# Kernel tuning notes

Hardware: AMD Instinct MI355X
Metric: run time of the kernel (lower is better)

Reference implementation:

```python
import jax, jax.numpy as jnp
import numpy as np

B, C, H, W = 16, 256, 56, 56
G, K, R = 16, 3, 2
CR = C // R          # reduced channels = 128
KKG = K * K * G      # span output channels = 144
EPS = 1e-5


def setup_inputs() -> dict:
    key = jax.random.key(0)
    ks = jax.random.split(key, 5)
    return {
        "x": jax.random.normal(ks[0], (B, C, H, W), jnp.float32),
        "w_reduce": jax.random.normal(ks[1], (CR, C), jnp.float32) * 0.05,
        "b_reduce": jax.random.normal(ks[2], (CR,), jnp.float32) * 0.05,
        "gamma": jnp.ones((CR,), jnp.float32),
        "beta": jnp.zeros((CR,), jnp.float32),
        "w_span": jax.random.normal(ks[3], (KKG, CR), jnp.float32) * 0.05,
        "b_span": jax.random.normal(ks[4], (KKG,), jnp.float32) * 0.05,
    }


def _conv1x1(x, w, bias):
    # 1x1 conv == channel contraction
    return jnp.einsum('bchw,oc->bohw', x, w) + bias[None, :, None, None]


def _involution(x, w_reduce, b_reduce, gamma, beta, w_span, b_span):
    b, c, h, w = x.shape
    # kernel-generation branch: reduce -> BN (batch stats) -> ReLU -> span
    t = _conv1x1(x, w_reduce, b_reduce)
    mu = t.mean(axis=(0, 2, 3), keepdims=True)
    var = t.var(axis=(0, 2, 3), keepdims=True)  # biased, as torch BN training
    t = (t - mu) * jax.lax.rsqrt(var + EPS)
    t = t * gamma[None, :, None, None] + beta[None, :, None, None]
    t = jax.nn.relu(t)
    kern = _conv1x1(t, w_span, b_span)  # [b, k*k*g, h, w]
    # 'b (k j g) h w -> b g (k j) h w'
    kern = kern.reshape(b, K, K, G, h, w).transpose(0, 3, 1, 2, 4, 5)
    kern = kern.reshape(b, G, K * K, h, w)
    # unfold x into [b, g, d, k*k, h, w] via shifted padded slices (no dense im2col buffer write pattern beyond necessity)
    p = K // 2
    xp = jnp.pad(x, ((0, 0), (0, 0), (p, p), (p, p)))
    patches = jnp.stack(
        [xp[:, :, i:i + h, j:j + w] for i in range(K) for j in range(K)],
        axis=2)  # [b, c, k*k, h, w]
    patches = patches.reshape(b, G, c // G, K * K, h, w)
    out = jnp.einsum('bgdxhw,bgxhw->bgdhw', patches, kern)  # weighted window sum
    return out.reshape(b, c, h, w)


def reference(x, w_reduce, b_reduce, gamma, beta, w_span, b_span):
    return _involution(x, w_reduce, b_reduce, gamma, beta, w_span, b_span)
```

## Files before the change

### kernel.cpp

```cpp
#include <hip/hip_runtime.h>

#define B_   16
#define C_   256
#define HW_  3136
#define W_   56
#define CR_  128
#define KKG_ 144
#define G_   16
#define NPOS (B_*HW_)
#define EPS_ 1e-5f
#define NBLK 784

typedef float f32x4 __attribute__((ext_vector_type(4)));
typedef short s16x8 __attribute__((ext_vector_type(8)));
typedef short s16x4 __attribute__((ext_vector_type(4)));

#define T2_OFF_B    0
#define KERN_OFF_B  12845056
#define GP_OFF_B    27295744
#define STAT_OFF_B  28098560
#define WBFR_OFF_B  28099584
#define WBFS_OFF_B  28165120

__device__ inline unsigned short f2bf(float f) {
    unsigned u = __float_as_uint(f);
    u += 0x7fff + ((u >> 16) & 1);
    return (unsigned short)(u >> 16);
}
__device__ inline float bf2f(unsigned short h) {
    return __uint_as_float(((unsigned)h) << 16);
}

__global__ __launch_bounds__(256) void prep_cast(
    const float* __restrict__ w_reduce, const float* __restrict__ w_span,
    unsigned short* __restrict__ wbfr, unsigned short* __restrict__ wbfs)
{
    int idx = blockIdx.x * 256 + threadIdx.x;
    if (idx < 32768) {
        wbfr[idx] = f2bf(w_reduce[idx]);
    } else {
        int k = idx - 32768;
        if (k < 18432) wbfs[k] = f2bf(w_span[k]);
    }
}

__global__ __launch_bounds__(256) void reduce_mfma(
    const float* __restrict__ x, const unsigned short* __restrict__ wbfr,
    unsigned short* __restrict__ t2, float* __restrict__ gp)
{
    __shared__ __align__(16) short as_[128 * 40];
    __shared__ __align__(16) short bs_[64 * 40];
    __shared__ float redp[128][2], redq[128][2];

    const int tid = threadIdx.x;
    const int lane = tid & 63, wv = tid >> 6;
    const int q = lane >> 4, i = lane & 15;
    const int mrow = (wv >> 1) * 64, nrow = (wv & 1) * 32;
    const int blk = blockIdx.x;
    const int b = blk / 49;
    const int p0 = (blk % 49) * 64;

    const float* xb = x + (size_t)b * C_ * HW_ + p0;

    const int o_a = tid >> 1, half = tid & 1;
    const int cp = tid >> 4, rq = tid & 15;

    f32x4 acc[4][2] = {};

    for (int c0 = 0; c0 < C_; c0 += 32) {
        {
            const unsigned short* src = wbfr + o_a * C_ + c0 + half * 16;
            s16x8 w0 = *(const s16x8*)src;
            s16x8 w1 = *(const s16x8*)(src + 8);
            *(s16x8*)&as_[o_a * 40 + half * 16] = w0;
            *(s16x8*)&as_[o_a * 40 + half * 16 + 8] = w1;
        }
        {
            const float* s0 = xb + (size_t)(c0 + 2 * cp) * HW_ + rq * 4;
            float4 va = *(const float4*)s0;
            float4 vb = *(const float4*)(s0 + HW_);
            float a4[4] = {va.x, va.y, va.z, va.w};
            float b4[4] = {vb.x, vb.y, vb.z, vb.w};
            #pragma unroll
            for (int j = 0; j < 4; j++) {
                unsigned pk = (unsigned)f2bf(a4[j]) | ((unsigned)f2bf(b4[j]) << 16);
                *(unsigned*)&bs_[(rq * 4 + j) * 40 + 2 * cp] = pk;
            }
        }
        __syncthreads();
        s16x8 af[4], bfr[2];
        #pragma unroll
        for (int mt = 0; mt < 4; mt++)
            af[mt] = *(const s16x8*)&as_[(mrow + mt * 16 + i) * 40 + q * 8];
        #pragma unroll
        for (int nt = 0; nt < 2; nt++)
            bfr[nt] = *(const s16x8*)&bs_[(nrow + nt * 16 + i) * 40 + q * 8];
        #pragma unroll
        for (int mt = 0; mt < 4; mt++)
            #pragma unroll
            for (int nt = 0; nt < 2; nt++)
                acc[mt][nt] = __builtin_amdgcn_mfma_f32_16x16x32_bf16(
                    af[mt], bfr[nt], acc[mt][nt], 0, 0, 0);
        __syncthreads();
    }

    #pragma unroll
    for (int mt = 0; mt < 4; mt++) {
        #pragma unroll
        for (int nt = 0; nt < 2; nt++) {
            #pragma unroll
            for (int reg = 0; reg < 4; reg++) {
                int o = mrow + mt * 16 + q * 4 + reg;
                int p = p0 + nrow + nt * 16 + i;
                t2[((size_t)o * B_ + b) * HW_ + p] = f2bf(acc[mt][nt][reg]);
            }
        }
        #pragma unroll
        for (int reg = 0; reg < 4; reg++) {
            float v0 = acc[mt][0][reg], v1 = acc[mt][1][reg];
            float s = v0 + v1;
            float ss = v0 * v0 + v1 * v1;
            #pragma unroll
            for (int m = 1; m < 16; m <<= 1) {
                s  += __shfl_xor(s, m);
                ss += __shfl_xor(ss, m);
            }
            if (i == 0) {
                int o = mrow + mt * 16 + q * 4 + reg;
                redp[o][wv & 1] = s;
                redq[o][wv & 1] = ss;
            }
        }
    }
    __syncthreads();
    if (tid < 128)
        gp[(size_t)blk * 256 + tid] = redp[tid][0] + redp[tid][1];
    else
        gp[(size_t)blk * 256 + tid] = redq[tid - 128][0] + redq[tid - 128][1];
}

__global__ __launch_bounds__(256) void bn_finalize(
    const float* __restrict__ gp, const float* __restrict__ gamma,
    const float* __restrict__ beta, float* __restrict__ stats)
{
    const int o = blockIdx.x;
    const int tid = threadIdx.x;
    float s = 0.f, ss = 0.f;
    for (int blk = tid; blk < NBLK; blk += 256) {
        s  += gp[(size_t)blk * 256 + o];
        ss += gp[(size_t)blk * 256 + 128 + o];
    }
    #pragma unroll
    for (int m = 1; m < 64; m <<= 1) {
        s  += __shfl_xor(s, m);
        ss += __shfl_xor(ss, m);
    }
    __shared__ float rs[4], rss[4];
    if ((tid & 63) == 0) { rs[tid >> 6] = s; rss[tid >> 6] = ss; }
    __syncthreads();
    if (tid == 0) {
        s  = rs[0] + rs[1] + rs[2] + rs[3];
        ss = rss[0] + rss[1] + rss[2] + rss[3];
        float inv_n = 1.0f / (float)NPOS;
        float mu = s * inv_n;
        float var = ss * inv_n - mu * mu;
        float sc = gamma[o] * rsqrtf(var + EPS_);
        stats[o] = sc;
        stats[128 + o] = beta[o] - mu * sc;
    }
}

__global__ __launch_bounds__(256) void span_mfma(
    const unsigned short* __restrict__ t2, const unsigned short* __restrict__ wbfs,
    const float* __restrict__ b_span, const float* __restrict__ stats,
    unsigned short* __restrict__ kern)
{
    __shared__ __align__(16) short as_[144 * 40];
    __shared__ __align__(16) short bs_[64 * 40];
    __shared__ float scs[128], shs[128], bsp[144];

    const int tid = threadIdx.x;
    const int lane = tid & 63, wv = tid >> 6;
    const int q = lane >> 4, i = lane & 15;
    const int blk = blockIdx.x;
    const int b = blk / 49;
    const int p0 = (blk % 49) * 64;

    if (tid < 128) { scs[tid] = stats[tid]; shs[tid] = stats[128 + tid]; }
    if (tid < 144) bsp[tid] = b_span[tid];
    __syncthreads();

    const int op = tid >> 4, seg = tid & 15;

    f32x4 acc[9] = {};

    for (int c0 = 0; c0 < CR_; c0 += 32) {
        #pragma unroll
        for (int P = 0; P < 3; P++) {
            int idx = P * 256 + tid;
            if (idx < 576) {
                int row = idx >> 2, k8 = idx & 3;
                *(s16x8*)&as_[row * 40 + k8 * 8] =
                    *(const s16x8*)&wbfs[row * CR_ + c0 + k8 * 8];
            }
        }
        {
            int cA = c0 + 2 * op;
            const unsigned short* tA = t2 + ((size_t)cA * B_ + b) * HW_ + p0 + seg * 4;
            s16x4 vA = *(const s16x4*)tA;
            s16x4 vB = *(const s16x4*)(tA + (size_t)B_ * HW_);
            float sA = scs[cA], hA = shs[cA];
            float sB = scs[cA + 1], hB = shs[cA + 1];
            #pragma unroll
            for (int j = 0; j < 4; j++) {
                float fa = fmaxf(fmaf(bf2f((unsigned short)vA[j]), sA, hA), 0.0f);
                float fb = fmaxf(fmaf(bf2f((unsigned short)vB[j]), sB, hB), 0.0f);
                unsigned pk = (unsigned)f2bf(fa) | ((unsigned)f2bf(fb) << 16);
                *(unsigned*)&bs_[(seg * 4 + j) * 40 + 2 * op] = pk;
            }
        }
        __syncthreads();
        s16x8 bfrag = *(const s16x8*)&bs_[(wv * 16 + i) * 40 + q * 8];
        #pragma unroll
        for (int mt = 0; mt < 9; mt++) {
            s16x8 af = *(const s16x8*)&as_[(mt * 16 + i) * 40 + q * 8];
            acc[mt] = __builtin_amdgcn_mfma_f32_16x16x32_bf16(af, bfrag, acc[mt], 0, 0, 0);
        }
        __syncthreads();
    }

    const int p = p0 + wv * 16 + i;
    #pragma unroll
    for (int mt = 0; mt < 9; mt++) {
        #pragma unroll
        for (int reg = 0; reg < 4; reg++) {
            int o2 = mt * 16 + q * 4 + reg;
            kern[((size_t)b * KKG_ + o2) * HW_ + p] = f2bf(acc[mt][reg] + bsp[o2]);
        }
    }
}

__global__ __launch_bounds__(256) void involution_apply(
    const float* __restrict__ x, const unsigned short* __restrict__ kern,
    float* __restrict__ out)
{
    int gtid = blockIdx.x * 256 + threadIdx.x;
    int pix = gtid % HW_;
    int bg  = gtid / HW_;
    int g = bg & 15;
    int b = bg >> 4;
    int h = pix / W_;
    int w = pix % W_;

    const unsigned short* kb = kern + (size_t)b * KKG_ * HW_ + pix;
    float kv[9];
    #pragma unroll
    for (int kk = 0; kk < 9; kk++)
        kv[kk] = bf2f(kb[(size_t)(kk * G_ + g) * HW_]);

    float acc[16];
    #pragma unroll
    for (int d = 0; d < 16; d++) acc[d] = 0.0f;

    const float* xb = x + (size_t)(b * C_ + g * 16) * HW_;
    #pragma unroll
    for (int di = 0; di < 3; di++) {
        int hh = h + di - 1;
        if (hh < 0 || hh >= W_) continue;
        #pragma unroll
        for (int dj = 0; dj < 3; dj++) {
            int ww = w + dj - 1;
            if (ww < 0 || ww >= W_) continue;
            float kval = kv[di * 3 + dj];
            int off = hh * W_ + ww;
            #pragma unroll
            for (int d = 0; d < 16; d++)
                acc[d] = fmaf(xb[(size_t)d * HW_ + off], kval, acc[d]);
        }
    }
    float* ob = out + (size_t)(b * C_ + g * 16) * HW_ + pix;
    #pragma unroll
    for (int d = 0; d < 16; d++) ob[(size_t)d * HW_] = acc[d];
}

extern "C" void kernel_launch(void* const* d_in, const int* in_sizes, int n_in,
                              void* d_out, int out_size, void* d_ws, size_t ws_size,
                              hipStream_t stream) {
    const float* x        = (const float*)d_in[0];
    const float* w_reduce = (const float*)d_in[1];
    const float* gamma    = (const float*)d_in[3];
    const float* beta     = (const float*)d_in[4];
    const float* w_span   = (const float*)d_in[5];
    const float* b_span   = (const float*)d_in[6];
    float* out = (float*)d_out;

    char* wsb = (char*)d_ws;
    unsigned short* t2   = (unsigned short*)(wsb + T2_OFF_B);
    unsigned short* kern = (unsigned short*)(wsb + KERN_OFF_B);
    float*          gp    = (float*)(wsb + GP_OFF_B);
    float*          stats = (float*)(wsb + STAT_OFF_B);
    unsigned short* wbfr = (unsigned short*)(wsb + WBFR_OFF_B);
    unsigned short* wbfs = (unsigned short*)(wsb + WBFS_OFF_B);

    prep_cast<<<200, 256, 0, stream>>>(w_reduce, w_span, wbfr, wbfs);
    reduce_mfma<<<NBLK, 256, 0, stream>>>(x, wbfr, t2, gp);
    bn_finalize<<<128, 256, 0, stream>>>(gp, gamma, beta, stats);
    span_mfma<<<NBLK, 256, 0, stream>>>(t2, wbfs, b_span, stats, kern);
    involution_apply<<<(B_ * G_ * HW_) / 256, 256, 0, stream>>>(x, kern, out);
}
```

Measured before the change: 161.5 us.

## Fuse span conv with involution apply via LDS-resident generated kernels

Merges the span MFMA kernel and the involution apply kernel into one. Generated per-pixel kernel weights are staged in shared memory as bf16 instead of being written to and re-read from a global buffer, and each block applies them across all 16 groups for its 64 pixels. This removes one launch and the global round trip of the kern tensor. In exchange it adds LDS use, which may lower occupancy, and the apply phase now runs with only 784 blocks, each thread looping over 4 groups.

```diff
diff --git a/kernel.cpp b/kernel.cpp
--- a/kernel.cpp
+++ b/kernel.cpp
@@ -16,7 +16,6 @@
 typedef short s16x4 __attribute__((ext_vector_type(4)));
 
 #define T2_OFF_B    0
-#define KERN_OFF_B  12845056
 #define GP_OFF_B    27295744
 #define STAT_OFF_B  28098560
 #define WBFR_OFF_B  28099584
@@ -170,13 +169,14 @@
     }
 }
 
-__global__ __launch_bounds__(256) void span_mfma(
+__global__ __launch_bounds__(256) void span_apply(
     const unsigned short* __restrict__ t2, const unsigned short* __restrict__ wbfs,
     const float* __restrict__ b_span, const float* __restrict__ stats,
-    unsigned short* __restrict__ kern)
+    const float* __restrict__ x, float* __restrict__ out)
 {
     __shared__ __align__(16) short as_[144 * 40];
     __shared__ __align__(16) short bs_[64 * 40];
+    __shared__ unsigned short klds[144 * 68];
     __shared__ float scs[128], shs[128], bsp[144];
 
     const int tid = threadIdx.x;
@@ -229,58 +229,60 @@
         __syncthreads();
     }
 
-    const int p = p0 + wv * 16 + i;
-    #pragma unroll
-    for (int mt = 0; mt < 9; mt++) {
-        #pragma unroll
-        for (int reg = 0; reg < 4; reg++) {
-            int o2 = mt * 16 + q * 4 + reg;
-            kern[((size_t)b * KKG_ + o2) * HW_ + p] = f2bf(acc[mt][reg] + bsp[o2]);
-        }
-    }
-}
-
-__global__ __launch_bounds__(256) void involution_apply(
-    const float* __restrict__ x, const unsigned short* __restrict__ kern,
-    float* __restrict__ out)
-{
-    int gtid = blockIdx.x * 256 + threadIdx.x;
-    int pix = gtid % HW_;
-    int bg  = gtid / HW_;
-    int g = bg & 15;
-    int b = bg >> 4;
-    int h = pix / W_;
-    int w = pix % W_;
-
-    const unsigned short* kb = kern + (size_t)b * KKG_ * HW_ + pix;
-    float kv[9];
-    #pragma unroll
-    for (int kk = 0; kk < 9; kk++)
-        kv[kk] = bf2f(kb[(size_t)(kk * G_ + g) * HW_]);
-
-    float acc[16];
-    #pragma unroll
-    for (int d = 0; d < 16; d++) acc[d] = 0.0f;
-
-    const float* xb = x + (size_t)(b * C_ + g * 16) * HW_;
-    #pragma unroll
-    for (int di = 0; di < 3; di++) {
-        int hh = h + di - 1;
-        if (hh < 0 || hh >= W_) continue;
-        #pragma unroll
-        for (int dj = 0; dj < 3; dj++) {
-            int ww = w + dj - 1;
-            if (ww < 0 || ww >= W_) continue;
-            float kval = kv[di * 3 + dj];
-            int off = hh * W_ + ww;
+    {
+        const int pl = wv * 16 + i;
+        #pragma unroll
+        for (int mt = 0; mt < 9; mt++) {
+            #pragma unroll
+            for (int reg = 0; reg < 4; reg++) {
+                int o2 = mt * 16 + q * 4 + reg;
+                klds[o2 * 68 + pl] = f2bf(acc[mt][reg] + bsp[o2]);
+            }
+        }
+    }
+    __syncthreads();
+
+    {
+        const int pl = tid & 63;
+        const int gq = tid >> 6;
+        const int p = p0 + pl;
+        const int h = p / W_, w = p % W_;
+        const float* xb = x + (size_t)b * C_ * HW_;
+        float* ob = out + (size_t)b * C_ * HW_ + p;
+
+        #pragma unroll
+        for (int gi = 0; gi < 4; gi++) {
+            const int g = gq * 4 + gi;
+            float kv[9];
+            #pragma unroll
+            for (int kk = 0; kk < 9; kk++)
+                kv[kk] = bf2f(klds[(kk * G_ + g) * 68 + pl]);
+
+            float a2[16];
+            #pragma unroll
+            for (int d = 0; d < 16; d++) a2[d] = 0.0f;
+
+            const float* xc = xb + (size_t)(g * 16) * HW_;
+            #pragma unroll
+            for (int di = 0; di < 3; di++) {
+                int hh = h + di - 1;
+                if (hh < 0 || hh >= W_) continue;
+                #pragma unroll
+                for (int dj = 0; dj < 3; dj++) {
+                    int ww = w + dj - 1;
+                    if (ww < 0 || ww >= W_) continue;
+                    float kval = kv[di * 3 + dj];
+                    int off = hh * W_ + ww;
+                    #pragma unroll
+                    for (int d = 0; d < 16; d++)
+                        a2[d] = fmaf(xc[(size_t)d * HW_ + off], kval, a2[d]);
+                }
+            }
             #pragma unroll
             for (int d = 0; d < 16; d++)
-                acc[d] = fmaf(xb[(size_t)d * HW_ + off], kval, acc[d]);
-        }
-    }
-    float* ob = out + (size_t)(b * C_ + g * 16) * HW_ + pix;
-    #pragma unroll
-    for (int d = 0; d < 16; d++) ob[(size_t)d * HW_] = acc[d];
+                ob[(size_t)(g * 16 + d) * HW_] = a2[d];
+        }
+    }
 }
 
 extern "C" void kernel_launch(void* const* d_in, const int* in_sizes, int n_in,
@@ -296,7 +298,6 @@
 
     char* wsb = (char*)d_ws;
     unsigned short* t2   = (unsigned short*)(wsb + T2_OFF_B);
-    unsigned short* kern = (unsigned short*)(wsb + KERN_OFF_B);
     float*          gp    = (float*)(wsb + GP_OFF_B);
     float*          stats = (float*)(wsb + STAT_OFF_B);
     unsigned short* wbfr = (unsigned short*)(wsb + WBFR_OFF_B);
@@ -305,6 +306,5 @@
     prep_cast<<<200, 256, 0, stream>>>(w_reduce, w_span, wbfr, wbfs);
     reduce_mfma<<<NBLK, 256, 0, stream>>>(x, wbfr, t2, gp);
     bn_finalize<<<128, 256, 0, stream>>>(gp, gamma, beta, stats);
-    span_mfma<<<NBLK, 256, 0, stream>>>(t2, wbfs, b_span, stats, kern);
-    involution_apply<<<(B_ * G_ * HW_) / 256, 256, 0, stream>>>(x, kern, out);
-}
+    span_apply<<<NBLK, 256, 0, stream>>>(t2, wbfs, b_span, stats, x, out);
+}
```

Result: slower. 180.0 us (+11.5%).

## Fuse weight bf16 cast into GEMM kernels and remap staging loads

Applied to the files above, without the earlier changes.

Removes the separate prep_cast launch and converts fp32 weights to bf16 inside reduce_mfma and span_mfma while staging tiles into shared memory. The B-tile staging is remapped so each lane loads one position across 8 channels and writes a single 16-byte LDS vector, replacing scattered 4-byte stores. The per-block BN partial sums are stored channel-major so bn_finalize reads them contiguously. The trade is redundant weight conversion in every block and double the weight read bytes, in exchange for one fewer launch and better LDS/global access patterns.

```diff
diff --git a/kernel.cpp b/kernel.cpp
--- a/kernel.cpp
+++ b/kernel.cpp
@@ -13,14 +13,11 @@
 
 typedef float f32x4 __attribute__((ext_vector_type(4)));
 typedef short s16x8 __attribute__((ext_vector_type(8)));
-typedef short s16x4 __attribute__((ext_vector_type(4)));
 
 #define T2_OFF_B    0
 #define KERN_OFF_B  12845056
 #define GP_OFF_B    27295744
 #define STAT_OFF_B  28098560
-#define WBFR_OFF_B  28099584
-#define WBFS_OFF_B  28165120
 
 __device__ inline unsigned short f2bf(float f) {
     unsigned u = __float_as_uint(f);
@@ -30,22 +27,12 @@
 __device__ inline float bf2f(unsigned short h) {
     return __uint_as_float(((unsigned)h) << 16);
 }
-
-__global__ __launch_bounds__(256) void prep_cast(
-    const float* __restrict__ w_reduce, const float* __restrict__ w_span,
-    unsigned short* __restrict__ wbfr, unsigned short* __restrict__ wbfs)
-{
-    int idx = blockIdx.x * 256 + threadIdx.x;
-    if (idx < 32768) {
-        wbfr[idx] = f2bf(w_reduce[idx]);
-    } else {
-        int k = idx - 32768;
-        if (k < 18432) wbfs[k] = f2bf(w_span[k]);
-    }
+__device__ inline unsigned pk2(float a, float b) {
+    return (unsigned)f2bf(a) | ((unsigned)f2bf(b) << 16);
 }
 
 __global__ __launch_bounds__(256) void reduce_mfma(
-    const float* __restrict__ x, const unsigned short* __restrict__ wbfr,
+    const float* __restrict__ x, const float* __restrict__ w_reduce,
     unsigned short* __restrict__ t2, float* __restrict__ gp)
 {
     __shared__ __align__(16) short as_[128 * 40];
@@ -61,31 +48,34 @@
     const int p0 = (blk % 49) * 64;
 
     const float* xb = x + (size_t)b * C_ * HW_ + p0;
-
     const int o_a = tid >> 1, half = tid & 1;
-    const int cp = tid >> 4, rq = tid & 15;
 
     f32x4 acc[4][2] = {};
 
     for (int c0 = 0; c0 < C_; c0 += 32) {
         {
-            const unsigned short* src = wbfr + o_a * C_ + c0 + half * 16;
-            s16x8 w0 = *(const s16x8*)src;
-            s16x8 w1 = *(const s16x8*)(src + 8);
-            *(s16x8*)&as_[o_a * 40 + half * 16] = w0;
-            *(s16x8*)&as_[o_a * 40 + half * 16 + 8] = w1;
+            const float* src = w_reduce + o_a * C_ + c0 + half * 16;
+            float4 f0 = ((const float4*)src)[0];
+            float4 f1 = ((const float4*)src)[1];
+            float4 f2v = ((const float4*)src)[2];
+            float4 f3 = ((const float4*)src)[3];
+            union { s16x8 v; unsigned u[4]; } W0, W1;
+            W0.u[0] = pk2(f0.x, f0.y);  W0.u[1] = pk2(f0.z, f0.w);
+            W0.u[2] = pk2(f1.x, f1.y);  W0.u[3] = pk2(f1.z, f1.w);
+            W1.u[0] = pk2(f2v.x, f2v.y); W1.u[1] = pk2(f2v.z, f2v.w);
+            W1.u[2] = pk2(f3.x, f3.y);  W1.u[3] = pk2(f3.z, f3.w);
+            *(s16x8*)&as_[o_a * 40 + half * 16] = W0.v;
+            *(s16x8*)&as_[o_a * 40 + half * 16 + 8] = W1.v;
         }
         {
-            const float* s0 = xb + (size_t)(c0 + 2 * cp) * HW_ + rq * 4;
-            float4 va = *(const float4*)s0;
-            float4 vb = *(const float4*)(s0 + HW_);
-            float a4[4] = {va.x, va.y, va.z, va.w};
-            float b4[4] = {vb.x, vb.y, vb.z, vb.w};
-            #pragma unroll
-            for (int j = 0; j < 4; j++) {
-                unsigned pk = (unsigned)f2bf(a4[j]) | ((unsigned)f2bf(b4[j]) << 16);
-                *(unsigned*)&bs_[(rq * 4 + j) * 40 + 2 * cp] = pk;
-            }
+            const float* sx = xb + (size_t)(c0 + (wv << 3)) * HW_ + lane;
+            float xv[8];
+            #pragma unroll
+            for (int k = 0; k < 8; k++) xv[k] = sx[(size_t)k * HW_];
+            union { s16x8 v; unsigned u[4]; } Bv;
+            #pragma unroll
+            for (int k = 0; k < 4; k++) Bv.u[k] = pk2(xv[2*k], xv[2*k+1]);
+            *(s16x8*)&bs_[lane * 40 + (wv << 3)] = Bv.v;
         }
         __syncthreads();
         s16x8 af[4], bfr[2];
@@ -134,9 +124,9 @@
     }
     __syncthreads();
     if (tid < 128)
-        gp[(size_t)blk * 256 + tid] = redp[tid][0] + redp[tid][1];
+        gp[(size_t)tid * NBLK + blk] = redp[tid][0] + redp[tid][1];
     else
-        gp[(size_t)blk * 256 + tid] = redq[tid - 128][0] + redq[tid - 128][1];
+        gp[(size_t)tid * NBLK + blk] = redq[tid - 128][0] + redq[tid - 128][1];
 }
 
 __global__ __launch_bounds__(256) void bn_finalize(
@@ -146,9 +136,9 @@
     const int o = blockIdx.x;
     const int tid = threadIdx.x;
     float s = 0.f, ss = 0.f;
-    for (int blk = tid; blk < NBLK; blk += 256) {
-        s  += gp[(size_t)blk * 256 + o];
-        ss += gp[(size_t)blk * 256 + 128 + o];
+    for (int idx = tid; idx < NBLK; idx += 256) {
+        s  += gp[(size_t)o * NBLK + idx];
+        ss += gp[(size_t)(128 + o) * NBLK + idx];
     }
     #pragma unroll
     for (int m = 1; m < 64; m <<= 1) {
@@ -171,7 +161,7 @@
 }
 
 __global__ __launch_bounds__(256) void span_mfma(
-    const unsigned short* __restrict__ t2, const unsigned short* __restrict__ wbfs,
+    const unsigned short* __restrict__ t2, const float* __restrict__ w_span,
     const float* __restrict__ b_span, const float* __restrict__ stats,
     unsigned short* __restrict__ kern)
 {
@@ -190,8 +180,6 @@
     if (tid < 144) bsp[tid] = b_span[tid];
     __syncthreads();
 
-    const int op = tid >> 4, seg = tid & 15;
-
     f32x4 acc[9] = {};
 
     for (int c0 = 0; c0 < CR_; c0 += 32) {
@@ -200,24 +188,29 @@
             int idx = P * 256 + tid;
             if (idx < 576) {
                 int row = idx >> 2, k8 = idx & 3;
-                *(s16x8*)&as_[row * 40 + k8 * 8] =
-                    *(const s16x8*)&wbfs[row * CR_ + c0 + k8 * 8];
+                const float* src = w_span + row * CR_ + c0 + k8 * 8;
+                float4 f0 = ((const float4*)src)[0];
+                float4 f1 = ((const float4*)src)[1];
+                union { s16x8 v; unsigned u[4]; } W0;
+                W0.u[0] = pk2(f0.x, f0.y);  W0.u[1] = pk2(f0.z, f0.w);
+                W0.u[2] = pk2(f1.x, f1.y);  W0.u[3] = pk2(f1.z, f1.w);
+                *(s16x8*)&as_[row * 40 + k8 * 8] = W0.v;
             }
         }
         {
-            int cA = c0 + 2 * op;
-            const unsigned short* tA = t2 + ((size_t)cA * B_ + b) * HW_ + p0 + seg * 4;
-            s16x4 vA = *(const s16x4*)tA;
-            s16x4 vB = *(const s16x4*)(tA + (size_t)B_ * HW_);
-            float sA = scs[cA], hA = shs[cA];
-            float sB = scs[cA + 1], hB = shs[cA + 1];
-            #pragma unroll
-            for (int j = 0; j < 4; j++) {
-                float fa = fmaxf(fmaf(bf2f((unsigned short)vA[j]), sA, hA), 0.0f);
-                float fb = fmaxf(fmaf(bf2f((unsigned short)vB[j]), sB, hB), 0.0f);
-                unsigned pk = (unsigned)f2bf(fa) | ((unsigned)f2bf(fb) << 16);
-                *(unsigned*)&bs_[(seg * 4 + j) * 40 + 2 * op] = pk;
-            }
+            const int cbase = c0 + (wv << 3);
+            const unsigned short* tsrc =
+                t2 + ((size_t)cbase * B_ + b) * HW_ + p0 + lane;
+            float fv[8];
+            #pragma unroll
+            for (int k = 0; k < 8; k++) {
+                float t = bf2f(tsrc[(size_t)k * B_ * HW_]);
+                fv[k] = fmaxf(fmaf(t, scs[cbase + k], shs[cbase + k]), 0.0f);
+            }
+            union { s16x8 v; unsigned u[4]; } Bv;
+            #pragma unroll
+            for (int k = 0; k < 4; k++) Bv.u[k] = pk2(fv[2*k], fv[2*k+1]);
+            *(s16x8*)&bs_[lane * 40 + (wv << 3)] = Bv.v;
         }
         __syncthreads();
         s16x8 bfrag = *(const s16x8*)&bs_[(wv * 16 + i) * 40 + q * 8];
@@ -299,12 +292,9 @@
     unsigned short* kern = (unsigned short*)(wsb + KERN_OFF_B);
     float*          gp    = (float*)(wsb + GP_OFF_B);
     float*          stats = (float*)(wsb + STAT_OFF_B);
-    unsigned short* wbfr = (unsigned short*)(wsb + WBFR_OFF_B);
-    unsigned short* wbfs = (unsigned short*)(wsb + WBFS_OFF_B);
-
-    prep_cast<<<200, 256, 0, stream>>>(w_reduce, w_span, wbfr, wbfs);
-    reduce_mfma<<<NBLK, 256, 0, stream>>>(x, wbfr, t2, gp);
+
+    reduce_mfma<<<NBLK, 256, 0, stream>>>(x, w_reduce, t2, gp);
     bn_finalize<<<128, 256, 0, stream>>>(gp, gamma, beta, stats);
-    span_mfma<<<NBLK, 256, 0, stream>>>(t2, wbfs, b_span, stats, kern);
+    span_mfma<<<NBLK, 256, 0, stream>>>(t2, w_span, b_span, stats, kern);
     involution_apply<<<(B_ * G_ * HW_) / 256, 256, 0, stream>>>(x, kern, out);
 }
```

Measured after the change: 165.6 us. 1.03x slower.

## Drop LDS staging in 1x1 GEMMs, use channel-last t2, atomic BN stats

Applied to the files above, without the earlier changes.

Both MFMA GEMM kernels now load operand fragments straight from global memory into registers instead of staging through shared memory with barriers. The intermediate t2 is stored position-major with channels innermost, so span_mfma can read 8 contiguous bf16 channels per lane. BN statistics are accumulated with atomicAdd into a small buffer zeroed in prep_cast, and the finalize step is folded into span_mfma, removing one kernel launch. The trade-off is that reduce_mfma reads x with strided scalar loads (each lane reads a different channel plane) and some global loads are duplicated across waves. The atomics also make the summation order nondeterministic.

```diff
diff --git a/kernel.cpp b/kernel.cpp
--- a/kernel.cpp
+++ b/kernel.cpp
@@ -13,14 +13,12 @@
 
 typedef float f32x4 __attribute__((ext_vector_type(4)));
 typedef short s16x8 __attribute__((ext_vector_type(8)));
-typedef short s16x4 __attribute__((ext_vector_type(4)));
 
 #define T2_OFF_B    0
 #define KERN_OFF_B  12845056
-#define GP_OFF_B    27295744
-#define STAT_OFF_B  28098560
-#define WBFR_OFF_B  28099584
-#define WBFS_OFF_B  28165120
+#define GACC_OFF_B  27295744
+#define WBFR_OFF_B  27296768
+#define WBFS_OFF_B  27362304
 
 __device__ inline unsigned short f2bf(float f) {
     unsigned u = __float_as_uint(f);
@@ -30,12 +28,17 @@
 __device__ inline float bf2f(unsigned short h) {
     return __uint_as_float(((unsigned)h) << 16);
 }
+__device__ inline unsigned pk2(float a, float b) {
+    return (unsigned)f2bf(a) | ((unsigned)f2bf(b) << 16);
+}
 
 __global__ __launch_bounds__(256) void prep_cast(
     const float* __restrict__ w_reduce, const float* __restrict__ w_span,
-    unsigned short* __restrict__ wbfr, unsigned short* __restrict__ wbfs)
+    unsigned short* __restrict__ wbfr, unsigned short* __restrict__ wbfs,
+    float* __restrict__ gacc)
 {
     int idx = blockIdx.x * 256 + threadIdx.x;
+    if (idx < 256) gacc[idx] = 0.0f;
     if (idx < 32768) {
         wbfr[idx] = f2bf(w_reduce[idx]);
     } else {
@@ -46,10 +49,8 @@
 
 __global__ __launch_bounds__(256) void reduce_mfma(
     const float* __restrict__ x, const unsigned short* __restrict__ wbfr,
-    unsigned short* __restrict__ t2, float* __restrict__ gp)
-{
-    __shared__ __align__(16) short as_[128 * 40];
-    __shared__ __align__(16) short bs_[64 * 40];
+    unsigned short* __restrict__ t2, float* __restrict__ gacc)
+{
     __shared__ float redp[128][2], redq[128][2];
 
     const int tid = threadIdx.x;
@@ -60,60 +61,49 @@
     const int b = blk / 49;
     const int p0 = (blk % 49) * 64;
 
-    const float* xb = x + (size_t)b * C_ * HW_ + p0;
-
-    const int o_a = tid >> 1, half = tid & 1;
-    const int cp = tid >> 4, rq = tid & 15;
+    const float* xpl = x + (size_t)b * C_ * HW_ + p0 + nrow + i;
+    const unsigned short* wb = wbfr + (size_t)(mrow + i) * C_ + q * 8;
 
     f32x4 acc[4][2] = {};
 
+    #pragma unroll
     for (int c0 = 0; c0 < C_; c0 += 32) {
-        {
-            const unsigned short* src = wbfr + o_a * C_ + c0 + half * 16;
-            s16x8 w0 = *(const s16x8*)src;
-            s16x8 w1 = *(const s16x8*)(src + 8);
-            *(s16x8*)&as_[o_a * 40 + half * 16] = w0;
-            *(s16x8*)&as_[o_a * 40 + half * 16 + 8] = w1;
-        }
-        {
-            const float* s0 = xb + (size_t)(c0 + 2 * cp) * HW_ + rq * 4;
-            float4 va = *(const float4*)s0;
-            float4 vb = *(const float4*)(s0 + HW_);
-            float a4[4] = {va.x, va.y, va.z, va.w};
-            float b4[4] = {vb.x, vb.y, vb.z, vb.w};
-            #pragma unroll
-            for (int j = 0; j < 4; j++) {
-                unsigned pk = (unsigned)f2bf(a4[j]) | ((unsigned)f2bf(b4[j]) << 16);
-                *(unsigned*)&bs_[(rq * 4 + j) * 40 + 2 * cp] = pk;
+        s16x8 af[4];
+        #pragma unroll
+        for (int mt = 0; mt < 4; mt++)
+            af[mt] = *(const s16x8*)(wb + (size_t)mt * 16 * C_ + c0);
+
+        s16x8 bfr[2];
+        #pragma unroll
+        for (int nt = 0; nt < 2; nt++) {
+            const float* xc = xpl + nt * 16;
+            union { s16x8 v; unsigned u[4]; } Bv;
+            #pragma unroll
+            for (int k2 = 0; k2 < 4; k2++) {
+                float fa = xc[(size_t)(c0 + q * 8 + 2 * k2) * HW_];
+                float fb = xc[(size_t)(c0 + q * 8 + 2 * k2 + 1) * HW_];
+                Bv.u[k2] = pk2(fa, fb);
             }
-        }
-        __syncthreads();
-        s16x8 af[4], bfr[2];
-        #pragma unroll
-        for (int mt = 0; mt < 4; mt++)
-            af[mt] = *(const s16x8*)&as_[(mrow + mt * 16 + i) * 40 + q * 8];
-        #pragma unroll
-        for (int nt = 0; nt < 2; nt++)
-            bfr[nt] = *(const s16x8*)&bs_[(nrow + nt * 16 + i) * 40 + q * 8];
+            bfr[nt] = Bv.v;
+        }
+
         #pragma unroll
         for (int mt = 0; mt < 4; mt++)
             #pragma unroll
             for (int nt = 0; nt < 2; nt++)
                 acc[mt][nt] = __builtin_amdgcn_mfma_f32_16x16x32_bf16(
                     af[mt], bfr[nt], acc[mt][nt], 0, 0, 0);
-        __syncthreads();
     }
 
     #pragma unroll
     for (int mt = 0; mt < 4; mt++) {
         #pragma unroll
         for (int nt = 0; nt < 2; nt++) {
-            #pragma unroll
-            for (int reg = 0; reg < 4; reg++) {
-                int o = mrow + mt * 16 + q * 4 + reg;
-                int p = p0 + nrow + nt * 16 + i;
-                t2[((size_t)o * B_ + b) * HW_ + p] = f2bf(acc[mt][nt][reg]);
-            }
+            int p = p0 + nrow + nt * 16 + i;
+            uint2 pr;
+            pr.x = pk2(acc[mt][nt][0], acc[mt][nt][1]);
+            pr.y = pk2(acc[mt][nt][2], acc[mt][nt][3]);
+            *(uint2*)(t2 + ((size_t)b * HW_ + p) * CR_ + mrow + mt * 16 + q * 4) = pr;
         }
         #pragma unroll
         for (int reg = 0; reg < 4; reg++) {
@@ -133,51 +123,18 @@
         }
     }
     __syncthreads();
-    if (tid < 128)
-        gp[(size_t)blk * 256 + tid] = redp[tid][0] + redp[tid][1];
-    else
-        gp[(size_t)blk * 256 + tid] = redq[tid - 128][0] + redq[tid - 128][1];
-}
-
-__global__ __launch_bounds__(256) void bn_finalize(
-    const float* __restrict__ gp, const float* __restrict__ gamma,
-    const float* __restrict__ beta, float* __restrict__ stats)
-{
-    const int o = blockIdx.x;
-    const int tid = threadIdx.x;
-    float s = 0.f, ss = 0.f;
-    for (int blk = tid; blk < NBLK; blk += 256) {
-        s  += gp[(size_t)blk * 256 + o];
-        ss += gp[(size_t)blk * 256 + 128 + o];
-    }
-    #pragma unroll
-    for (int m = 1; m < 64; m <<= 1) {
-        s  += __shfl_xor(s, m);
-        ss += __shfl_xor(ss, m);
-    }
-    __shared__ float rs[4], rss[4];
-    if ((tid & 63) == 0) { rs[tid >> 6] = s; rss[tid >> 6] = ss; }
-    __syncthreads();
-    if (tid == 0) {
-        s  = rs[0] + rs[1] + rs[2] + rs[3];
-        ss = rss[0] + rss[1] + rss[2] + rss[3];
-        float inv_n = 1.0f / (float)NPOS;
-        float mu = s * inv_n;
-        float var = ss * inv_n - mu * mu;
-        float sc = gamma[o] * rsqrtf(var + EPS_);
-        stats[o] = sc;
-        stats[128 + o] = beta[o] - mu * sc;
-    }
+    if (tid < 128) atomicAdd(&gacc[tid], redp[tid][0] + redp[tid][1]);
+    else           atomicAdd(&gacc[tid], redq[tid - 128][0] + redq[tid - 128][1]);
 }
 
 __global__ __launch_bounds__(256) void span_mfma(
     const unsigned short* __restrict__ t2, const unsigned short* __restrict__ wbfs,
-    const float* __restrict__ b_span, const float* __restrict__ stats,
+    const float* __restrict__ b_span, const float* __restrict__ gacc,
+    const float* __restrict__ gamma, const float* __restrict__ beta,
     unsigned short* __restrict__ kern)
 {
-    __shared__ __align__(16) short as_[144 * 40];
-    __shared__ __align__(16) short bs_[64 * 40];
-    __shared__ float scs[128], shs[128], bsp[144];
+    __shared__ __align__(16) float scs[128], shs[128];
+    __shared__ float bsp[144];
 
     const int tid = threadIdx.x;
     const int lane = tid & 63, wv = tid >> 6;
@@ -186,50 +143,53 @@
     const int b = blk / 49;
     const int p0 = (blk % 49) * 64;
 
-    if (tid < 128) { scs[tid] = stats[tid]; shs[tid] = stats[128 + tid]; }
+    if (tid < 128) {
+        float s = gacc[tid], ss = gacc[128 + tid];
+        const float inv_n = 1.0f / (float)NPOS;
+        float mu = s * inv_n;
+        float var = ss * inv_n - mu * mu;
+        float sc = gamma[tid] * rsqrtf(var + EPS_);
+        scs[tid] = sc;
+        shs[tid] = beta[tid] - mu * sc;
+    }
     if (tid < 144) bsp[tid] = b_span[tid];
     __syncthreads();
 
-    const int op = tid >> 4, seg = tid & 15;
+    const int p = p0 + wv * 16 + i;
+    const unsigned short* tb = t2 + ((size_t)b * HW_ + p) * CR_ + q * 8;
+    const unsigned short* wb = wbfs + (size_t)i * CR_ + q * 8;
 
     f32x4 acc[9] = {};
 
+    #pragma unroll
     for (int c0 = 0; c0 < CR_; c0 += 32) {
-        #pragma unroll
-        for (int P = 0; P < 3; P++) {
-            int idx = P * 256 + tid;
-            if (idx < 576) {
-                int row = idx >> 2, k8 = idx & 3;
-                *(s16x8*)&as_[row * 40 + k8 * 8] =
-                    *(const s16x8*)&wbfs[row * CR_ + c0 + k8 * 8];
-            }
-        }
-        {
-            int cA = c0 + 2 * op;
-            const unsigned short* tA = t2 + ((size_t)cA * B_ + b) * HW_ + p0 + seg * 4;
-            s16x4 vA = *(const s16x4*)tA;
-            s16x4 vB = *(const s16x4*)(tA + (size_t)B_ * HW_);
-            float sA = scs[cA], hA = shs[cA];
-            float sB = scs[cA + 1], hB = shs[cA + 1];
-            #pragma unroll
-            for (int j = 0; j < 4; j++) {
-                float fa = fmaxf(fmaf(bf2f((unsigned short)vA[j]), sA, hA), 0.0f);
-                float fb = fmaxf(fmaf(bf2f((unsigned short)vB[j]), sB, hB), 0.0f);
-                unsigned pk = (unsigned)f2bf(fa) | ((unsigned)f2bf(fb) << 16);
-                *(unsigned*)&bs_[(seg * 4 + j) * 40 + 2 * op] = pk;
-            }
-        }
-        __syncthreads();
-        s16x8 bfrag = *(const s16x8*)&bs_[(wv * 16 + i) * 40 + q * 8];
+        const int cb = c0 + q * 8;
+        s16x8 traw = *(const s16x8*)(tb + c0);
+        float4 s0 = *(const float4*)&scs[cb];
+        float4 s1 = *(const float4*)&scs[cb + 4];
+        float4 h0 = *(const float4*)&shs[cb];
+        float4 h1 = *(const float4*)&shs[cb + 4];
+        float f0 = fmaxf(fmaf(bf2f((unsigned short)traw[0]), s0.x, h0.x), 0.f);
+        float f1 = fmaxf(fmaf(bf2f((unsigned short)traw[1]), s0.y, h0.y), 0.f);
+        float f2 = fmaxf(fmaf(bf2f((unsigned short)traw[2]), s0.z, h0.z), 0.f);
+        float f3 = fmaxf(fmaf(bf2f((unsigned short)traw[3]), s0.w, h0.w), 0.f);
+        float f4 = fmaxf(fmaf(bf2f((unsigned short)traw[4]), s1.x, h1.x), 0.f);
+        float f5 = fmaxf(fmaf(bf2f((unsigned short)traw[5]), s1.y, h1.y), 0.f);
+        float f6 = fmaxf(fmaf(bf2f((unsigned short)traw[6]), s1.z, h1.z), 0.f);
+        float f7 = fmaxf(fmaf(bf2f((unsigned short)traw[7]), s1.w, h1.w), 0.f);
+        union { s16x8 v; unsigned u[4]; } Bv;
+        Bv.u[0] = pk2(f0, f1);
+        Bv.u[1] = pk2(f2, f3);
+        Bv.u[2] = pk2(f4, f5);
+        Bv.u[3] = pk2(f6, f7);
+
         #pragma unroll
         for (int mt = 0; mt < 9; mt++) {
-            s16x8 af = *(const s16x8*)&as_[(mt * 16 + i) * 40 + q * 8];
-            acc[mt] = __builtin_amdgcn_mfma_f32_16x16x32_bf16(af, bfrag, acc[mt], 0, 0, 0);
-        }
-        __syncthreads();
-    }
-
-    const int p = p0 + wv * 16 + i;
+            s16x8 af = *(const s16x8*)(wb + (size_t)mt * 16 * CR_ + c0);
+            acc[mt] = __builtin_amdgcn_mfma_f32_16x16x32_bf16(af, Bv.v, acc[mt], 0, 0, 0);
+        }
+    }
+
     #pragma unroll
     for (int mt = 0; mt < 9; mt++) {
         #pragma unroll
@@ -297,14 +257,12 @@
     char* wsb = (char*)d_ws;
     unsigned short* t2   = (unsigned short*)(wsb + T2_OFF_B);
     unsigned short* kern = (unsigned short*)(wsb + KERN_OFF_B);
-    float*          gp    = (float*)(wsb + GP_OFF_B);
-    float*          stats = (float*)(wsb + STAT_OFF_B);
+    float*          gacc = (float*)(wsb + GACC_OFF_B);
     unsigned short* wbfr = (unsigned short*)(wsb + WBFR_OFF_B);
     unsigned short* wbfs = (unsigned short*)(wsb + WBFS_OFF_B);
 
-    prep_cast<<<200, 256, 0, stream>>>(w_reduce, w_span, wbfr, wbfs);
-    reduce_mfma<<<NBLK, 256, 0, stream>>>(x, wbfr, t2, gp);
-    bn_finalize<<<128, 256, 0, stream>>>(gp, gamma, beta, stats);
-    span_mfma<<<NBLK, 256, 0, stream>>>(t2, wbfs, b_span, stats, kern);
+    prep_cast<<<200, 256, 0, stream>>>(w_reduce, w_span, wbfr, wbfs, gacc);
+    reduce_mfma<<<NBLK, 256, 0, stream>>>(x, wbfr, t2, gacc);
+    span_mfma<<<NBLK, 256, 0, stream>>>(t2, wbfs, b_span, gacc, gamma, beta, kern);
     involution_apply<<<(B_ * G_ * HW_) / 256, 256, 0, stream>>>(x, kern, out);
 }
```

After: 191.2 us. 18.4% more time.
